# Optimization experiments

Hardware: AMD Instinct MI355X
Metric: run time of the kernel (lower is better)

The kernel has to match this reference:

```python
import jax, jax.numpy as jnp
import numpy as np

N = 50000
E = 800000
D = 128
LN_EPS = 1e-5


def setup_inputs() -> dict:
    key = jax.random.key(0)
    ks = jax.random.split(key, 12)
    s = 1.0 / np.sqrt(D)
    return {
        "x": jax.random.normal(ks[0], (N, D), dtype=jnp.float32),
        "edge_index": jax.random.randint(ks[1], (2, E), 0, N, dtype=jnp.int64),
        "edge_attr": jax.random.normal(ks[2], (E, D), dtype=jnp.float32),
        # GINEConv edge projection Linear(edge_dim=D, in_channels=D)
        "Wl": jax.random.uniform(ks[3], (D, D), jnp.float32, -s, s),
        "bl": jax.random.uniform(ks[4], (D,), jnp.float32, -s, s),
        # mlp: Linear(D,D) -> ReLU -> Linear(D,D)
        "W1": jax.random.uniform(ks[5], (D, D), jnp.float32, -s, s),
        "b1": jax.random.uniform(ks[6], (D,), jnp.float32, -s, s),
        "W2": jax.random.uniform(ks[7], (D, D), jnp.float32, -s, s),
        "b2": jax.random.uniform(ks[8], (D,), jnp.float32, -s, s),
        # PyG LayerNorm affine
        "ln_w": jnp.ones((D,), jnp.float32),
        "ln_b": jnp.zeros((D,), jnp.float32),
    }


def reference(x, edge_index, edge_attr, Wl, bl, W1, b1, W2, b2, ln_w, ln_b):
    src = edge_index[0]  # j (message source)
    dst = edge_index[1]  # i (aggregation target)
    # GINEConv message: ReLU(x_j + lin(edge_attr)) -- gather + elementwise
    e = edge_attr @ Wl + bl                      # [E, D]
    msg = jax.nn.relu(x[src] + e)                # [E, D]
    # scatter-sum aggregation into destination nodes
    agg = jax.ops.segment_sum(msg, dst, num_segments=N)  # [N, D]
    # eps = 0 (train_eps=False): nn((1+eps)*x + agg)
    h = x + agg
    h = jax.nn.relu(h @ W1 + b1) @ W2 + b2       # MLP
    # residual
    h = h + x
    # PyG LayerNorm, mode='graph', batch=None: normalize over all entries
    mu = jnp.mean(h)
    std = jnp.sqrt(jnp.mean((h - mu) ** 2))
    h = (h - mu) / (std + LN_EPS) * ln_w + ln_b
    # SiLU, dropout(eval)=identity, nan_to_num
    h = jax.nn.silu(h)
    return jnp.nan_to_num(h)
```

## Files before the change

### kernel.cpp

```cpp
#include <hip/hip_runtime.h>
#include <math.h>

#define NN 50000
#define EE 800000
#define D128 128
#define LN_EPSF 1e-5f

#define NBK 12500
#define CAP 128

typedef __bf16 bf16_t;
typedef __bf16 bf16x8 __attribute__((ext_vector_type(8)));
typedef float f32x4 __attribute__((ext_vector_type(4)));

#define AGG_F (NN * D128)

__device__ __forceinline__ bf16x8 cvt8(float4 f0, float4 f1) {
    bf16x8 r;
    r[0] = (bf16_t)f0.x; r[1] = (bf16_t)f0.y; r[2] = (bf16_t)f0.z; r[3] = (bf16_t)f0.w;
    r[4] = (bf16_t)f1.x; r[5] = (bf16_t)f1.y; r[6] = (bf16_t)f1.z; r[7] = (bf16_t)f1.w;
    return r;
}

__device__ __forceinline__ bf16x8 zero8() {
    bf16x8 z;
    #pragma unroll
    for (int j = 0; j < 8; ++j) z[j] = (bf16_t)0.f;
    return z;
}

__device__ __forceinline__ void load_w_lds(const float* __restrict__ W, bf16_t* Wlds,
                                           const float* __restrict__ bias, float* b_s) {
    int tid = threadIdx.x;
    for (int i = tid; i < D128 * D128; i += 256) {
        int k = i >> 7, n = i & 127;
        Wlds[(n * D128 + k) ^ ((n & 7) << 3)] = (bf16_t)W[i];
    }
    if (tid < D128) b_s[tid] = bias[tid];
    __syncthreads();
}

__global__ __launch_bounds__(256) void k_zero0(int* __restrict__ cursor,
                                               float* __restrict__ sc,
                                               const int* __restrict__ ei32,
                                               int* __restrict__ flag) {
    const int idx = blockIdx.x * 256 + threadIdx.x;
    if (blockIdx.x == 0 && threadIdx.x < 64) {
        unsigned long long m = __ballot(ei32[2 * threadIdx.x + 1] == 0);
        if (threadIdx.x == 0) { flag[0] = (m == ~0ULL) ? 1 : 0; sc[0] = 0.f; sc[1] = 0.f; }
    }
    for (int i = idx; i < NBK; i += gridDim.x * 256) cursor[i] = 0;
}

__device__ __forceinline__ void idx_pair(const void* ei, int is64, int e, int& sj, int& di) {
    if (is64) {
        const long long* p = (const long long*)ei;
        sj = (int)p[e]; di = (int)p[EE + e];
    } else {
        const int* p = (const int*)ei;
        sj = p[e]; di = p[EE + e];
    }
}

__global__ __launch_bounds__(256) void k_scatter(const void* __restrict__ eidx,
                                                 const int* __restrict__ flag,
                                                 int* __restrict__ cursor,
                                                 int2* __restrict__ entries) {
    const int is64 = flag[0];
    for (int e = blockIdx.x * 256 + threadIdx.x; e < EE; e += gridDim.x * 256) {
        int sj, di;
        idx_pair(eidx, is64, e, sj, di);
        const int b = di >> 2;
        const int dl = di & 3;
        const int p = atomicAdd(&cursor[b], 1);
        if (p < CAP) entries[(size_t)b * CAP + p] = make_int2(e, (dl << 16) | sj);
    }
}

__global__ __launch_bounds__(256) void k_bagg(
    const float* __restrict__ ea, const float* __restrict__ x,
    const float* __restrict__ Wl, const float* __restrict__ bl,
    const int2* __restrict__ entries, const int* __restrict__ cursor,
    float* __restrict__ agg)
{
    __shared__ bf16_t Wlds[D128 * D128];
    __shared__ float bl_s[D128];
    load_w_lds(Wl, Wlds, bl, bl_s);

    const int lane = threadIdx.x & 63, wid = threadIdx.x >> 6;
    const int l15 = lane & 15, lg = lane >> 4;
    const int b = blockIdx.x * 4 + wid;

    bf16x8 id0 = zero8(), id1 = zero8();
    #pragma unroll
    for (int j = 0; j < 8; ++j) {
        if (8 * lg + j == l15)      id0[j] = (bf16_t)1.0f;
        if (8 * lg + j == l15 + 16) id1[j] = (bf16_t)1.0f;
    }
    float blv[8];
    #pragma unroll
    for (int q = 0; q < 8; ++q) blv[q] = bl_s[l15 + 16 * q];

    const int2* eb = entries + (size_t)b * CAP;
    const int cnt = min(cursor[b], CAP);
    int2 m0 = eb[lane];
    int2 m1 = eb[64 + lane];
    if (lane >= cnt)      m0 = make_int2(0, 0);
    if (64 + lane >= cnt) m1 = make_int2(0, 0);

    const int ntiles = (cnt + 15) >> 4;

    float ns0[8], ns1[8], ns2[8], ns3[8];
    #pragma unroll
    for (int q = 0; q < 8; ++q) { ns0[q] = 0.f; ns1[q] = 0.f; ns2[q] = 0.f; ns3[q] = 0.f; }

    for (int t = 0; t < ntiles; ++t) {
        const int sl = (t * 16 + l15) & 63;
        const bool lo = (t < 4);
        const int ex = lo ? __shfl(m0.x, sl) : __shfl(m1.x, sl);
        const int ey = lo ? __shfl(m0.y, sl) : __shfl(m1.y, sl);
        const int eid = ex;
        const int src = ey & 0xffff;

        int dlr[4];
        #pragma unroll
        for (int i = 0; i < 4; ++i) dlr[i] = (__shfl(ey, lg * 4 + i, 16) >> 16) & 3;

        float4 eF[8], xF[8];
        {
            const float* rp = ea + (size_t)eid * D128 + lg * 8;
            #pragma unroll
            for (int s = 0; s < 4; ++s) {
                eF[2 * s]     = *(const float4*)(rp + s * 32);
                eF[2 * s + 1] = *(const float4*)(rp + s * 32 + 4);
            }
            const float* xp = x + (size_t)src * D128 + lg * 8;
            #pragma unroll
            for (int s = 0; s < 4; ++s) {
                xF[2 * s]     = *(const float4*)(xp + s * 32);
                xF[2 * s + 1] = *(const float4*)(xp + s * 32 + 4);
            }
        }

        f32x4 acc[8];
        #pragma unroll
        for (int q = 0; q < 8; ++q) acc[q] = f32x4{0.f, 0.f, 0.f, 0.f};
        #pragma unroll
        for (int s = 0; s < 4; ++s) {
            const bf16x8 af = cvt8(eF[2 * s], eF[2 * s + 1]);
            const int kb = s * 32 + lg * 8;
            #pragma unroll
            for (int q = 0; q < 8; ++q) {
                const int col = l15 + 16 * q;
                bf16x8 bf = *(const bf16x8*)&Wlds[(col * D128 + kb) ^ ((col & 7) << 3)];
                acc[q] = __builtin_amdgcn_mfma_f32_16x16x32_bf16(af, bf, acc[q], 0, 0, 0);
            }
            const bf16x8 xf = cvt8(xF[2 * s], xF[2 * s + 1]);
            acc[2 * s]     = __builtin_amdgcn_mfma_f32_16x16x32_bf16(xf, id0, acc[2 * s], 0, 0, 0);
            acc[2 * s + 1] = __builtin_amdgcn_mfma_f32_16x16x32_bf16(xf, id1, acc[2 * s + 1], 0, 0, 0);
        }

        #pragma unroll
        for (int i = 0; i < 4; ++i) {
            const bool vr = (t * 16 + lg * 4 + i) < cnt;
            #pragma unroll
            for (int q = 0; q < 8; ++q) {
                float v = fmaxf(acc[q][i] + blv[q], 0.f);
                v = vr ? v : 0.f;
                ns0[q] += (dlr[i] == 0) ? v : 0.f;
                ns1[q] += (dlr[i] == 1) ? v : 0.f;
                ns2[q] += (dlr[i] == 2) ? v : 0.f;
                ns3[q] += (dlr[i] == 3) ? v : 0.f;
            }
        }
    }

    #pragma unroll
    for (int q = 0; q < 8; ++q) {
        ns0[q] += __shfl_xor(ns0[q], 16); ns0[q] += __shfl_xor(ns0[q], 32);
        ns1[q] += __shfl_xor(ns1[q], 16); ns1[q] += __shfl_xor(ns1[q], 32);
        ns2[q] += __shfl_xor(ns2[q], 16); ns2[q] += __shfl_xor(ns2[q], 32);
        ns3[q] += __shfl_xor(ns3[q], 16); ns3[q] += __shfl_xor(ns3[q], 32);
    }
    float* ag = agg + (size_t)(b * 4 + lg) * D128 + l15;
    if (lg == 0) {
        #pragma unroll
        for (int q = 0; q < 8; ++q) ag[16 * q] = ns0[q];
    } else if (lg == 1) {
        #pragma unroll
        for (int q = 0; q < 8; ++q) ag[16 * q] = ns1[q];
    } else if (lg == 2) {
        #pragma unroll
        for (int q = 0; q < 8; ++q) ag[16 * q] = ns2[q];
    } else {
        #pragma unroll
        for (int q = 0; q < 8; ++q) ag[16 * q] = ns3[q];
    }
}

__global__ __launch_bounds__(256) void k_mlp1(
    const float* __restrict__ x, const float* __restrict__ agg,
    const float* __restrict__ W1, const float* __restrict__ b1,
    float* __restrict__ tbuf)
{
    __shared__ bf16_t Wlds[D128 * D128];
    __shared__ float b_s[D128];
    load_w_lds(W1, Wlds, b1, b_s);

    const int lane = threadIdx.x & 63, wid = threadIdx.x >> 6;
    const int l15 = lane & 15, lg = lane >> 4;
    const int nbase = blockIdx.x * 64 + wid * 16;
    if (nbase >= NN) return;

    const int row = nbase + l15;
    bf16x8 a[4];
    if (row < NN) {
        const float* xr = x + (size_t)row * D128 + lg * 8;
        const float* gr = agg + (size_t)row * D128 + lg * 8;
        #pragma unroll
        for (int s = 0; s < 4; ++s) {
            float4 f0 = *(const float4*)(xr + s * 32);
            float4 f1 = *(const float4*)(xr + s * 32 + 4);
            float4 g0 = *(const float4*)(gr + s * 32);
            float4 g1 = *(const float4*)(gr + s * 32 + 4);
            float4 h0 = {f0.x + g0.x, f0.y + g0.y, f0.z + g0.z, f0.w + g0.w};
            float4 h1 = {f1.x + g1.x, f1.y + g1.y, f1.z + g1.z, f1.w + g1.w};
            a[s] = cvt8(h0, h1);
        }
    } else {
        #pragma unroll
        for (int s = 0; s < 4; ++s) a[s] = zero8();
    }
    f32x4 acc[8];
    #pragma unroll
    for (int t = 0; t < 8; ++t) acc[t] = f32x4{0.f, 0.f, 0.f, 0.f};
    #pragma unroll
    for (int s = 0; s < 4; ++s) {
        const int kb = s * 32 + lg * 8;
        #pragma unroll
        for (int t = 0; t < 8; ++t) {
            const int col = l15 + 16 * t;
            bf16x8 b = *(const bf16x8*)&Wlds[(col * D128 + kb) ^ ((col & 7) << 3)];
            acc[t] = __builtin_amdgcn_mfma_f32_16x16x32_bf16(a[s], b, acc[t], 0, 0, 0);
        }
    }
    #pragma unroll
    for (int i = 0; i < 4; ++i) {
        const int r = nbase + lg * 4 + i;
        if (r < NN) {
            float* tr = tbuf + (size_t)r * D128;
            #pragma unroll
            for (int t = 0; t < 8; ++t) {
                const int c = l15 + 16 * t;
                tr[c] = fmaxf(acc[t][i] + b_s[c], 0.0f);
            }
        }
    }
}

__global__ __launch_bounds__(256) void k_mlp2(
    const float* __restrict__ tbuf, const float* __restrict__ x,
    const float* __restrict__ W2, const float* __restrict__ b2,
    float* __restrict__ out, float* __restrict__ sc)
{
    __shared__ bf16_t Wlds[D128 * D128];
    __shared__ float b_s[D128];
    __shared__ float red[8];
    load_w_lds(W2, Wlds, b2, b_s);

    const int tid = threadIdx.x;
    const int lane = tid & 63, wid = tid >> 6;
    const int l15 = lane & 15, lg = lane >> 4;
    const int nbase = blockIdx.x * 64 + wid * 16;
    float s1 = 0.f, s2 = 0.f;

    if (nbase < NN) {
        const int row = nbase + l15;
        bf16x8 a[4];
        if (row < NN) {
            const float* rp = tbuf + (size_t)row * D128 + lg * 8;
            #pragma unroll
            for (int s = 0; s < 4; ++s) {
                float4 f0 = *(const float4*)(rp + s * 32);
                float4 f1 = *(const float4*)(rp + s * 32 + 4);
                a[s] = cvt8(f0, f1);
            }
        } else {
            #pragma unroll
            for (int s = 0; s < 4; ++s) a[s] = zero8();
        }
        f32x4 acc[8];
        #pragma unroll
        for (int t = 0; t < 8; ++t) acc[t] = f32x4{0.f, 0.f, 0.f, 0.f};
        #pragma unroll
        for (int s = 0; s < 4; ++s) {
            const int kb = s * 32 + lg * 8;
            #pragma unroll
            for (int t = 0; t < 8; ++t) {
                const int col = l15 + 16 * t;
                bf16x8 b = *(const bf16x8*)&Wlds[(col * D128 + kb) ^ ((col & 7) << 3)];
                acc[t] = __builtin_amdgcn_mfma_f32_16x16x32_bf16(a[s], b, acc[t], 0, 0, 0);
            }
        }
        #pragma unroll
        for (int i = 0; i < 4; ++i) {
            const int r = nbase + lg * 4 + i;
            if (r < NN) {
                #pragma unroll
                for (int t = 0; t < 8; ++t) {
                    const int c = l15 + 16 * t;
                    float v = acc[t][i] + b_s[c] + x[(size_t)r * D128 + c];
                    out[(size_t)r * D128 + c] = v;
                    s1 += v;
                    s2 += v * v;
                }
            }
        }
    }
    #pragma unroll
    for (int o = 32; o > 0; o >>= 1) {
        s1 += __shfl_xor(s1, o);
        s2 += __shfl_xor(s2, o);
    }
    if (lane == 0) { red[wid * 2] = s1; red[wid * 2 + 1] = s2; }
    __syncthreads();
    if (tid == 0) {
        float a1 = red[0] + red[2] + red[4] + red[6];
        float a2 = red[1] + red[3] + red[5] + red[7];
        unsafeAtomicAdd(&sc[0], a1);
        unsafeAtomicAdd(&sc[1], a2);
    }
}

__global__ __launch_bounds__(256) void k_ln(
    float* __restrict__ out, const float* __restrict__ sc,
    const float* __restrict__ lnw, const float* __restrict__ lnb)
{
    const float inv = 1.0f / (float)(NN * D128);
    const float mu = sc[0] * inv;
    const float var = sc[1] * inv - mu * mu;
    const float rstd = 1.0f / (sqrtf(fmaxf(var, 0.f)) + LN_EPSF);
    const int total = NN * D128 / 4;
    for (int idx = blockIdx.x * 256 + threadIdx.x; idx < total; idx += gridDim.x * 256) {
        float4 h = ((const float4*)out)[idx];
        const int c0 = (idx * 4) & 127;
        float4 w = *(const float4*)(lnw + c0);
        float4 bb = *(const float4*)(lnb + c0);
        float4 r;
        r.x = (h.x - mu) * rstd * w.x + bb.x;
        r.y = (h.y - mu) * rstd * w.y + bb.y;
        r.z = (h.z - mu) * rstd * w.z + bb.z;
        r.w = (h.w - mu) * rstd * w.w + bb.w;
        r.x = r.x / (1.f + __expf(-r.x));
        r.y = r.y / (1.f + __expf(-r.y));
        r.z = r.z / (1.f + __expf(-r.z));
        r.w = r.w / (1.f + __expf(-r.w));
        if (r.x != r.x) r.x = 0.f;
        if (r.y != r.y) r.y = 0.f;
        if (r.z != r.z) r.z = 0.f;
        if (r.w != r.w) r.w = 0.f;
        ((float4*)out)[idx] = r;
    }
}

extern "C" void kernel_launch(void* const* d_in, const int* in_sizes, int n_in,
                              void* d_out, int out_size, void* d_ws, size_t ws_size,
                              hipStream_t stream)
{
    const float* x   = (const float*)d_in[0];
    const void*  ei  = d_in[1];
    const float* ea  = (const float*)d_in[2];
    const float* Wl  = (const float*)d_in[3];
    const float* bl  = (const float*)d_in[4];
    const float* W1  = (const float*)d_in[5];
    const float* b1  = (const float*)d_in[6];
    const float* W2  = (const float*)d_in[7];
    const float* b2  = (const float*)d_in[8];
    const float* lnw = (const float*)d_in[9];
    const float* lnb = (const float*)d_in[10];
    float* out = (float*)d_out;

    float* agg = (float*)d_ws;
    float* sc  = agg + AGG_F;
    int* flag  = (int*)(sc + 2);

    int2* entries = (int2*)d_out;
    int* cursor   = (int*)(entries + (size_t)NBK * CAP);

    k_zero0<<<49, 256, 0, stream>>>(cursor, sc, (const int*)ei, flag);
    k_scatter<<<1024, 256, 0, stream>>>(ei, flag, cursor, entries);
    k_bagg<<<NBK / 4, 256, 0, stream>>>(ea, x, Wl, bl, entries, cursor, agg);
    k_mlp1<<<(NN + 63) / 64, 256, 0, stream>>>(x, agg, W1, b1, out);
    k_mlp2<<<(NN + 63) / 64, 256, 0, stream>>>(out, x, W2, b2, out, sc);
    k_ln<<<NN * D128 / 4 / 256, 256, 0, stream>>>(out, sc, lnw, lnb);
}
```

Baseline: 406.8 us.

## Restructure edge aggregation: 512-thread blocks, epilogue x add, per-tile reductions

k_bagg now runs 8 waves per block, so each LDS copy of the bf16 Wl matrix serves 8 destination buckets, and it asks for 4 blocks per CU. The identity-matrix MFMAs that folded x_src into the accumulators are removed; x is instead read with scalar loads and added in the bias/ReLU epilogue. The four per-destination partial-sum arrays become one array, reduced across lane groups with shuffles every tile. The intent is to cut register pressure and MFMA work to raise occupancy, at the cost of more shuffles per tile and less explicit load prefetching.

Result: slower. 777.4 us (+91.1%).

```diff
diff --git a/kernel.cpp b/kernel.cpp
--- a/kernel.cpp
+++ b/kernel.cpp
@@ -32,7 +32,8 @@
 __device__ __forceinline__ void load_w_lds(const float* __restrict__ W, bf16_t* Wlds,
                                            const float* __restrict__ bias, float* b_s) {
     int tid = threadIdx.x;
-    for (int i = tid; i < D128 * D128; i += 256) {
+    int nth = blockDim.x;
+    for (int i = tid; i < D128 * D128; i += nth) {
         int k = i >> 7, n = i & 127;
         Wlds[(n * D128 + k) ^ ((n & 7) << 3)] = (bf16_t)W[i];
     }
@@ -77,7 +78,7 @@
     }
 }
 
-__global__ __launch_bounds__(256) void k_bagg(
+__global__ __launch_bounds__(512, 4) void k_bagg(
     const float* __restrict__ ea, const float* __restrict__ x,
     const float* __restrict__ Wl, const float* __restrict__ bl,
     const int2* __restrict__ entries, const int* __restrict__ cursor,
@@ -89,14 +90,9 @@
 
     const int lane = threadIdx.x & 63, wid = threadIdx.x >> 6;
     const int l15 = lane & 15, lg = lane >> 4;
-    const int b = blockIdx.x * 4 + wid;
-
-    bf16x8 id0 = zero8(), id1 = zero8();
-    #pragma unroll
-    for (int j = 0; j < 8; ++j) {
-        if (8 * lg + j == l15)      id0[j] = (bf16_t)1.0f;
-        if (8 * lg + j == l15 + 16) id1[j] = (bf16_t)1.0f;
-    }
+    const int b = blockIdx.x * 8 + wid;
+    if (b >= NBK) return;
+
     float blv[8];
     #pragma unroll
     for (int q = 0; q < 8; ++q) blv[q] = bl_s[l15 + 16 * q];
@@ -110,9 +106,9 @@
 
     const int ntiles = (cnt + 15) >> 4;
 
-    float ns0[8], ns1[8], ns2[8], ns3[8];
-    #pragma unroll
-    for (int q = 0; q < 8; ++q) { ns0[q] = 0.f; ns1[q] = 0.f; ns2[q] = 0.f; ns3[q] = 0.f; }
+    float sum[8];
+    #pragma unroll
+    for (int q = 0; q < 8; ++q) sum[q] = 0.f;
 
     for (int t = 0; t < ntiles; ++t) {
         const int sl = (t * 16 + l15) & 63;
@@ -120,34 +116,23 @@
         const int ex = lo ? __shfl(m0.x, sl) : __shfl(m1.x, sl);
         const int ey = lo ? __shfl(m0.y, sl) : __shfl(m1.y, sl);
         const int eid = ex;
-        const int src = ey & 0xffff;
-
-        int dlr[4];
-        #pragma unroll
-        for (int i = 0; i < 4; ++i) dlr[i] = (__shfl(ey, lg * 4 + i, 16) >> 16) & 3;
-
-        float4 eF[8], xF[8];
-        {
-            const float* rp = ea + (size_t)eid * D128 + lg * 8;
-            #pragma unroll
-            for (int s = 0; s < 4; ++s) {
-                eF[2 * s]     = *(const float4*)(rp + s * 32);
-                eF[2 * s + 1] = *(const float4*)(rp + s * 32 + 4);
-            }
-            const float* xp = x + (size_t)src * D128 + lg * 8;
-            #pragma unroll
-            for (int s = 0; s < 4; ++s) {
-                xF[2 * s]     = *(const float4*)(xp + s * 32);
-                xF[2 * s + 1] = *(const float4*)(xp + s * 32 + 4);
-            }
+
+        int srcr[4], dlr[4];
+        #pragma unroll
+        for (int i = 0; i < 4; ++i) {
+            const int eyr = __shfl(ey, lg * 4 + i, 16);
+            srcr[i] = eyr & 0xffff;
+            dlr[i]  = (eyr >> 16) & 3;
         }
 
         f32x4 acc[8];
         #pragma unroll
         for (int q = 0; q < 8; ++q) acc[q] = f32x4{0.f, 0.f, 0.f, 0.f};
+        const float* rp = ea + (size_t)eid * D128 + lg * 8;
         #pragma unroll
         for (int s = 0; s < 4; ++s) {
-            const bf16x8 af = cvt8(eF[2 * s], eF[2 * s + 1]);
+            const bf16x8 af = cvt8(*(const float4*)(rp + s * 32),
+                                   *(const float4*)(rp + s * 32 + 4));
             const int kb = s * 32 + lg * 8;
             #pragma unroll
             for (int q = 0; q < 8; ++q) {
@@ -155,47 +140,35 @@
                 bf16x8 bf = *(const bf16x8*)&Wlds[(col * D128 + kb) ^ ((col & 7) << 3)];
                 acc[q] = __builtin_amdgcn_mfma_f32_16x16x32_bf16(af, bf, acc[q], 0, 0, 0);
             }
-            const bf16x8 xf = cvt8(xF[2 * s], xF[2 * s + 1]);
-            acc[2 * s]     = __builtin_amdgcn_mfma_f32_16x16x32_bf16(xf, id0, acc[2 * s], 0, 0, 0);
-            acc[2 * s + 1] = __builtin_amdgcn_mfma_f32_16x16x32_bf16(xf, id1, acc[2 * s + 1], 0, 0, 0);
         }
 
         #pragma unroll
         for (int i = 0; i < 4; ++i) {
             const bool vr = (t * 16 + lg * 4 + i) < cnt;
+            const float* xr = x + (size_t)srcr[i] * D128;
             #pragma unroll
             for (int q = 0; q < 8; ++q) {
-                float v = fmaxf(acc[q][i] + blv[q], 0.f);
-                v = vr ? v : 0.f;
-                ns0[q] += (dlr[i] == 0) ? v : 0.f;
-                ns1[q] += (dlr[i] == 1) ? v : 0.f;
-                ns2[q] += (dlr[i] == 2) ? v : 0.f;
-                ns3[q] += (dlr[i] == 3) ? v : 0.f;
-            }
-        }
-    }
-
-    #pragma unroll
-    for (int q = 0; q < 8; ++q) {
-        ns0[q] += __shfl_xor(ns0[q], 16); ns0[q] += __shfl_xor(ns0[q], 32);
-        ns1[q] += __shfl_xor(ns1[q], 16); ns1[q] += __shfl_xor(ns1[q], 32);
-        ns2[q] += __shfl_xor(ns2[q], 16); ns2[q] += __shfl_xor(ns2[q], 32);
-        ns3[q] += __shfl_xor(ns3[q], 16); ns3[q] += __shfl_xor(ns3[q], 32);
-    }
+                float v = fmaxf(acc[q][i] + blv[q] + xr[l15 + 16 * q], 0.f);
+                acc[q][i] = vr ? v : 0.f;
+            }
+        }
+        #pragma unroll
+        for (int d = 0; d < 4; ++d) {
+            #pragma unroll
+            for (int q = 0; q < 8; ++q) {
+                float p = 0.f;
+                #pragma unroll
+                for (int i = 0; i < 4; ++i) p += (dlr[i] == d) ? acc[q][i] : 0.f;
+                p += __shfl_xor(p, 16);
+                p += __shfl_xor(p, 32);
+                sum[q] += (lg == d) ? p : 0.f;
+            }
+        }
+    }
+
     float* ag = agg + (size_t)(b * 4 + lg) * D128 + l15;
-    if (lg == 0) {
-        #pragma unroll
-        for (int q = 0; q < 8; ++q) ag[16 * q] = ns0[q];
-    } else if (lg == 1) {
-        #pragma unroll
-        for (int q = 0; q < 8; ++q) ag[16 * q] = ns1[q];
-    } else if (lg == 2) {
-        #pragma unroll
-        for (int q = 0; q < 8; ++q) ag[16 * q] = ns2[q];
-    } else {
-        #pragma unroll
-        for (int q = 0; q < 8; ++q) ag[16 * q] = ns3[q];
-    }
+    #pragma unroll
+    for (int q = 0; q < 8; ++q) ag[16 * q] = sum[q];
 }
 
 __global__ __launch_bounds__(256) void k_mlp1(
@@ -389,7 +362,7 @@
 
     k_zero0<<<49, 256, 0, stream>>>(cursor, sc, (const int*)ei, flag);
     k_scatter<<<1024, 256, 0, stream>>>(ei, flag, cursor, entries);
-    k_bagg<<<NBK / 4, 256, 0, stream>>>(ea, x, Wl, bl, entries, cursor, agg);
+    k_bagg<<<(NBK + 7) / 8, 512, 0, stream>>>(ea, x, Wl, bl, entries, cursor, agg);
     k_mlp1<<<(NN + 63) / 64, 256, 0, stream>>>(x, agg, W1, b1, out);
     k_mlp2<<<(NN + 63) / 64, 256, 0, stream>>>(out, x, W2, b2, out, sc);
     k_ln<<<NN * D128 / 4 / 256, 256, 0, stream>>>(out, sc, lnw, lnb);
```
